# Optimization experiments

Hardware: AMD Instinct MI355X
Metric: run time of the kernel (lower is better)

## Reference

```python
import jax, jax.numpy as jnp
import numpy as np

D_MODEL = 1024
NUM_HEADS = 16


def setup_inputs() -> dict:
    key = jax.random.key(0)
    ks = jax.random.split(key, 5)
    sigma = (2.0 / (D_MODEL + D_MODEL)) ** 0.5
    def trunc(k):
        # truncated normal in [-3*sigma, 3*sigma], std sigma
        return sigma * jax.random.truncated_normal(k, -3.0, 3.0, (D_MODEL, D_MODEL), jnp.float32)
    x = jax.random.normal(ks[0], (4, 2048, D_MODEL), jnp.float32)
    return {
        "x": x,
        "W_Q": trunc(ks[1]),
        "W_K": trunc(ks[2]),
        "W_V": trunc(ks[3]),
        "W_O": trunc(ks[4]),
    }


def _mha(x, W_Q, W_K, W_V, W_O):
    B, S, D = x.shape
    H = NUM_HEADS
    dk = D // H
    # Linear stores W as (d_out, d_in); einsum '... d_in, d_out d_in -> ... d_out'
    Q = jnp.einsum('bsd,ed->bse', x, W_Q).reshape(B, S, H, dk).transpose(0, 2, 1, 3)
    K = jnp.einsum('bsd,ed->bse', x, W_K).reshape(B, S, H, dk).transpose(0, 2, 1, 3)
    V = jnp.einsum('bsd,ed->bse', x, W_V).reshape(B, S, H, dk).transpose(0, 2, 1, 3)
    scores = jnp.einsum('bhnd,bhmd->bhnm', Q, K) / jnp.sqrt(jnp.asarray(dk, x.dtype))
    causal = jnp.tril(jnp.ones((S, S), bool))
    scores = jnp.where(causal, scores, -jnp.inf)
    attn = jax.nn.softmax(scores, axis=-1)
    out = jnp.einsum('bhnm,bhmd->bhnd', attn, V)  # [B,H,S,dk]
    out = out.transpose(0, 2, 1, 3).reshape(B, S, D)
    return jnp.einsum('bsd,ed->bse', out, W_O)


def reference(x, W_Q, W_K, W_V, W_O):
    return _mha(x, W_Q, W_K, W_V, W_O)
```

## Files before the change

### kernel.cpp

```cpp
#include <hip/hip_runtime.h>
#include <hip/hip_bf16.h>
#include <stdint.h>


typedef unsigned short u16;
typedef short bf16x8 __attribute__((ext_vector_type(8)));
typedef float f32x4 __attribute__((ext_vector_type(4)));
typedef unsigned short u16x8 __attribute__((ext_vector_type(8)));

#define S_LEN 2048
#define DMODEL 1024
#define NH 16

__device__ __forceinline__ u16 f2bf(float f) {
    unsigned u = __builtin_bit_cast(unsigned, f);
    unsigned r = (u + 0x7fffu + ((u >> 16) & 1u)) >> 16;
    return (u16)r;
}

__device__ __forceinline__ float fast_exp2(float x) {
    return __builtin_amdgcn_exp2f(x);
}

__device__ __forceinline__ unsigned cvtpk_bf16(float lo, float hi_) {
    unsigned r;
    asm("v_cvt_pk_bf16_f32 %0, %1, %2" : "=v"(r) : "v"(lo), "v"(hi_));
    return r;
}

__device__ __forceinline__ void gll16(const void* g, void* s) {
    __builtin_amdgcn_global_load_lds((const __attribute__((address_space(1))) unsigned*)g,
                                     (__attribute__((address_space(3))) unsigned*)s, 16, 0, 0);
}

__global__ __launch_bounds__(256) void cast_all(
    const float* __restrict__ x, const float* __restrict__ wq, const float* __restrict__ wk,
    const float* __restrict__ wv, const float* __restrict__ wo,
    u16* __restrict__ xb, u16* __restrict__ wqkv, u16* __restrict__ wob, int nx) {
    const int NW = DMODEL * DMODEL;
    int i4 = (blockIdx.x * 256 + threadIdx.x) * 4;
    const float* src; u16* dst; int off;
    if (i4 < nx)             { src = x;  dst = xb;            off = i4; }
    else if (i4 < nx + NW)   { src = wq; dst = wqkv;          off = i4 - nx; }
    else if (i4 < nx + 2*NW) { src = wk; dst = wqkv + NW;     off = i4 - nx - NW; }
    else if (i4 < nx + 3*NW) { src = wv; dst = wqkv + 2*NW;   off = i4 - nx - 2*NW; }
    else                     { src = wo; dst = wob;           off = i4 - nx - 3*NW; }
    float4 v = *reinterpret_cast<const float4*>(src + off);
    ushort4 o4; o4.x = f2bf(v.x); o4.y = f2bf(v.y); o4.z = f2bf(v.z); o4.w = f2bf(v.w);
    *reinterpret_cast<ushort4*>(dst + off) = o4;
}

template <typename OUT>
__global__ __launch_bounds__(256) void gemm_bt(const u16* __restrict__ A, const u16* __restrict__ B,
                                               OUT* __restrict__ C, int M, int N, int K,
                                               int qcols, float qscale) {
    __shared__ u16 As[128 * 32];
    __shared__ u16 Bs[128 * 32];
    const int m0 = blockIdx.y * 128, n0 = blockIdx.x * 128;
    const int t = threadIdx.x, w = t >> 6, l = t & 63;
    const int wr = w >> 1, wc = w & 1;
    f32x4 acc[4][4] = {};

    const int srow = w * 16 + (l >> 2);
    const int scol = (l & 3) * 8;
    const u16* Ag = A + (size_t)(m0 + srow) * K + scol;
    const u16* Bg = B + (size_t)(n0 + srow) * K + scol;

    for (int k0 = 0; k0 < K; k0 += 32) {
        __syncthreads();
        gll16(Ag + k0,                  As + w * 512);
        gll16(Ag + (size_t)64 * K + k0, As + 2048 + w * 512);
        gll16(Bg + k0,                  Bs + w * 512);
        gll16(Bg + (size_t)64 * K + k0, Bs + 2048 + w * 512);
        __syncthreads();
        bf16x8 af[4], bfr[4];
#pragma unroll
        for (int mi = 0; mi < 4; mi++)
            af[mi] = *(const bf16x8*)&As[(wr * 64 + mi * 16 + (l & 15)) * 32 + (l >> 4) * 8];
#pragma unroll
        for (int ni = 0; ni < 4; ni++)
            bfr[ni] = *(const bf16x8*)&Bs[(wc * 64 + ni * 16 + (l & 15)) * 32 + (l >> 4) * 8];
#pragma unroll
        for (int mi = 0; mi < 4; mi++)
#pragma unroll
            for (int ni = 0; ni < 4; ni++)
                acc[mi][ni] = __builtin_amdgcn_mfma_f32_16x16x32_bf16(af[mi], bfr[ni], acc[mi][ni], 0, 0, 0);
    }
#pragma unroll
    for (int mi = 0; mi < 4; mi++)
#pragma unroll
        for (int ni = 0; ni < 4; ni++)
#pragma unroll
            for (int j = 0; j < 4; j++) {
                int r = m0 + wr * 64 + mi * 16 + (l >> 4) * 4 + j;
                int c = n0 + wc * 64 + ni * 16 + (l & 15);
                float v = acc[mi][ni][j];
                if (c < qcols) v *= qscale;
                if constexpr (__is_same(OUT, u16)) C[(size_t)r * N + c] = f2bf(v);
                else                               C[(size_t)r * N + c] = v;
            }
}

__global__ __launch_bounds__(256) void transpose_v(const u16* __restrict__ QKV, u16* __restrict__ VT) {
    __shared__ u16 tile[64 * 66];
    const int st = blockIdx.x, bh = blockIdx.y;
    const int b = bh >> 4, h = bh & 15;
    const int s0 = st * 64;
    const int t = threadIdx.x;
#pragma unroll
    for (int i = 0; i < 2; i++) {
        int cid = i * 256 + t;
        int srow = cid >> 3, c8 = cid & 7;
        u16x8 v = *(const u16x8*)&QKV[(size_t)(b * S_LEN + s0 + srow) * 3072 + 2048 + h * 64 + c8 * 8];
#pragma unroll
        for (int j = 0; j < 8; j++) tile[srow * 66 + c8 * 8 + j] = v[j];
    }
    __syncthreads();
#pragma unroll
    for (int i = 0; i < 2; i++) {
        int cid = i * 256 + t;
        int d = cid >> 3, sc8 = cid & 7;
        u16x8 o;
#pragma unroll
        for (int j = 0; j < 8; j++) o[j] = tile[(sc8 * 8 + j) * 66 + d];
        *(u16x8*)&VT[(size_t)(bh * 64 + d) * S_LEN + s0 + sc8 * 8] = o;
    }
}

__global__ __launch_bounds__(512, 4) void attn(const u16* __restrict__ QKV, const u16* __restrict__ VT,
                                               u16* __restrict__ O) {
    const int bh = blockIdx.x, p = blockIdx.y;
    const int b = bh >> 4, h = bh & 15;
    const int t = threadIdx.x, w = t >> 6, l = t & 63;
    const int q = l & 15, hi = l >> 4, s7 = q & 7;

    __shared__ u16 SM[2][2][64][64];
    __shared__ u16 PS[8][16][64];

    const int srow = t >> 3, sblk = t & 7;
    const int gs = (sblk ^ (srow & 7)) * 8;
    const u16* Kg = QKV + (size_t)(b * S_LEN + srow) * 3072 + 1024 + h * 64 + gs;
    const u16* Vg = VT + (size_t)(bh * 64 + srow) * S_LEN + gs;

    const int kA0 = q * 128 + ((hi ^ s7) << 4);
    const int kA1 = kA0 ^ 64;
    const char* smbase = (const char*)&SM[0][0][0][0];

    char* pbase = (char*)&PS[w][0][0];
    const int pw0 = q * 128 + ((((0 * 2) + (hi >> 1)) ^ s7) << 4) + ((hi & 1) << 3);
    const int pw1 = q * 128 + ((((1 * 2) + (hi >> 1)) ^ s7) << 4) + ((hi & 1) << 3);
    const int pw2 = q * 128 + ((((2 * 2) + (hi >> 1)) ^ s7) << 4) + ((hi & 1) << 3);
    const int pw3 = q * 128 + ((((3 * 2) + (hi >> 1)) ^ s7) << 4) + ((hi & 1) << 3);
    const int pr0 = q * 128 + (((0 * 4 + hi) ^ s7) << 4);
    const int pr1 = q * 128 + (((1 * 4 + hi) ^ s7) << 4);

#pragma unroll 1
    for (int part = 0; part < 2; ++part) {
        const int q128 = (part == 0 ? p : 15 - p) * 128;
        const int nt = q128 / 64 + 2;
        const int qglob = q128 + w * 16 + q;

        bf16x8 qf[2];
#pragma unroll
        for (int kk = 0; kk < 2; kk++)
            qf[kk] = *(const bf16x8*)&QKV[(size_t)(b * S_LEN + qglob) * 3072 + h * 64 + kk * 32 + hi * 8];

        f32x4 oacc[4] = {};
        float m_ = -1e30f, l_ = 0.f;

        gll16(Kg, (u16*)&SM[0][0][0][0] + t * 8);
        gll16(Vg, (u16*)&SM[0][1][0][0] + t * 8);
        __syncthreads();

        const u16* KgT = Kg + (size_t)64 * 3072;
        const u16* VgT = Vg + 64;

#pragma unroll 1
        for (int tt = 0; tt < nt; ++tt) {
            const int cur = tt & 1;
            if (tt + 1 < nt) {
                gll16(KgT, (u16*)&SM[cur ^ 1][0][0][0] + t * 8);
                gll16(VgT, (u16*)&SM[cur ^ 1][1][0][0] + t * 8);
                KgT += (size_t)64 * 3072;
                VgT += 64;
            }
            const int kv0 = tt * 64;
            if (q128 + w * 16 + 15 >= kv0) {
                const char* kb = smbase + cur * 16384;
                f32x4 sacc[4] = {};
#pragma unroll
                for (int kk = 0; kk < 2; kk++) {
                    const char* ka = kb + (kk ? kA1 : kA0);
#pragma unroll
                    for (int ni = 0; ni < 4; ni++) {
                        bf16x8 kf = *(const bf16x8*)(ka + ni * 2048);
                        sacc[ni] = __builtin_amdgcn_mfma_f32_16x16x32_bf16(kf, qf[kk], sacc[ni], 0, 0, 0);
                    }
                }
                const int r0 = qglob - kv0;
                if (r0 < 63) {
                    const int rth = r0 - hi * 4;
#pragma unroll
                    for (int ni = 0; ni < 4; ni++)
#pragma unroll
                        for (int j = 0; j < 4; j++)
                            if (ni * 16 + j > rth) sacc[ni][j] = -1e30f;
                }
                float x0 = fmaxf(fmaxf(sacc[0][0], sacc[0][1]), fmaxf(sacc[0][2], sacc[0][3]));
                float x1 = fmaxf(fmaxf(sacc[1][0], sacc[1][1]), fmaxf(sacc[1][2], sacc[1][3]));
                float x2 = fmaxf(fmaxf(sacc[2][0], sacc[2][1]), fmaxf(sacc[2][2], sacc[2][3]));
                float x3 = fmaxf(fmaxf(sacc[3][0], sacc[3][1]), fmaxf(sacc[3][2], sacc[3][3]));
                float pm = fmaxf(fmaxf(x0, x1), fmaxf(x2, x3));
                pm = fmaxf(pm, __shfl_xor(pm, 16, 64));
                pm = fmaxf(pm, __shfl_xor(pm, 32, 64));
                if (!__all(pm <= m_ + 8.0f)) {
                    float mnew = fmaxf(m_, pm);
                    float sc = fast_exp2(m_ - mnew);
                    m_ = mnew;
                    l_ *= sc;
#pragma unroll
                    for (int di = 0; di < 4; di++) oacc[di] *= sc;
                }
                float pv[4][4];
#pragma unroll
                for (int ni = 0; ni < 4; ni++)
#pragma unroll
                    for (int j = 0; j < 4; j++) pv[ni][j] = fast_exp2(sacc[ni][j] - m_);
                float ss = ((pv[0][0] + pv[0][1]) + (pv[0][2] + pv[0][3]))
                         + ((pv[1][0] + pv[1][1]) + (pv[1][2] + pv[1][3]))
                         + ((pv[2][0] + pv[2][1]) + (pv[2][2] + pv[2][3]))
                         + ((pv[3][0] + pv[3][1]) + (pv[3][2] + pv[3][3]));
                ss += __shfl_xor(ss, 16, 64);
                ss += __shfl_xor(ss, 32, 64);
                l_ += ss;
                *(uint2*)(pbase + pw0) = make_uint2(cvtpk_bf16(pv[0][0], pv[0][1]), cvtpk_bf16(pv[0][2], pv[0][3]));
                *(uint2*)(pbase + pw1) = make_uint2(cvtpk_bf16(pv[1][0], pv[1][1]), cvtpk_bf16(pv[1][2], pv[1][3]));
                *(uint2*)(pbase + pw2) = make_uint2(cvtpk_bf16(pv[2][0], pv[2][1]), cvtpk_bf16(pv[2][2], pv[2][3]));
                *(uint2*)(pbase + pw3) = make_uint2(cvtpk_bf16(pv[3][0], pv[3][1]), cvtpk_bf16(pv[3][2], pv[3][3]));
                bf16x8 pf0 = *(const bf16x8*)(pbase + pr0);
                bf16x8 pf1 = *(const bf16x8*)(pbase + pr1);
                const char* vb = kb + 8192;
#pragma unroll
                for (int kk = 0; kk < 2; kk++) {
                    const char* va = vb + (kk ? kA1 : kA0);
                    bf16x8 pf = kk ? pf1 : pf0;
#pragma unroll
                    for (int di = 0; di < 4; di++) {
                        bf16x8 vf = *(const bf16x8*)(va + di * 2048);
                        oacc[di] = __builtin_amdgcn_mfma_f32_16x16x32_bf16(vf, pf, oacc[di], 0, 0, 0);
                    }
                }
            }
            __syncthreads();
        }

        float inv = 1.0f / l_;
#pragma unroll
        for (int di = 0; di < 4; di++) {
            ushort4 o4;
            o4.x = f2bf(oacc[di][0] * inv);
            o4.y = f2bf(oacc[di][1] * inv);
            o4.z = f2bf(oacc[di][2] * inv);
            o4.w = f2bf(oacc[di][3] * inv);
            *(ushort4*)&O[(size_t)(b * S_LEN + qglob) * DMODEL + h * 64 + di * 16 + hi * 4] = o4;
        }
    }
}

extern "C" void kernel_launch(void* const* d_in, const int* in_sizes, int n_in,
                              void* d_out, int out_size, void* d_ws, size_t ws_size,
                              hipStream_t stream) {
    const float* x  = (const float*)d_in[0];
    const float* wq = (const float*)d_in[1];
    const float* wk = (const float*)d_in[2];
    const float* wv = (const float*)d_in[3];
    const float* wo = (const float*)d_in[4];
    const int nx = in_sizes[0];
    const int BS = nx / DMODEL;
    const int NW = DMODEL * DMODEL;

    u16* xb   = (u16*)d_ws;
    u16* wqkv = xb + (size_t)nx;
    u16* wob  = wqkv + (size_t)3 * NW;
    u16* qkv  = wob + (size_t)NW;
    u16* vt   = qkv + (size_t)BS * 3072;
    u16* ob   = vt + (size_t)nx;

    int ncast = (nx + 4 * NW) / 4 / 256;
    cast_all<<<ncast, 256, 0, stream>>>(x, wq, wk, wv, wo, xb, wqkv, wob, nx);

    const float QSC = 0.125f * 1.44269504088896f;
    gemm_bt<u16><<<dim3(3072 / 128, BS / 128), 256, 0, stream>>>(xb, wqkv, qkv, BS, 3072, DMODEL,
                                                                 DMODEL, QSC);

    transpose_v<<<dim3(S_LEN / 64, (BS / S_LEN) * NH), 256, 0, stream>>>(qkv, vt);

    attn<<<dim3((BS / S_LEN) * NH, 8), 512, 0, stream>>>(qkv, vt, ob);

    gemm_bt<float><<<dim3(DMODEL / 128, BS / 128), 256, 0, stream>>>(ob, wob, (float*)d_out, BS, DMODEL, DMODEL,
                                                                     0, 1.0f);
}
```

Measured before the change: 188.6 us.

## Fuse V transpose into QKV GEMM epilogue, widen GEMM K-tile with swizzle

The QKV GEMM now writes the V part directly in transposed layout through a small per-wave LDS staging buffer, which removes the separate transpose_v kernel and its extra read and write of V. The GEMM K-step grows from 32 to 64, with an XOR-swizzled LDS layout to avoid bank conflicts, halving the number of barrier pairs per tile. The attention kernel also wraps its MFMA blocks in s_setprio so those waves get issue priority. The costs are more LDS per GEMM block, which may lower occupancy, and the QKV buffer no longer holds V, which is fine because attention reads V only from vt.

```diff
diff --git a/kernel.cpp b/kernel.cpp
--- a/kernel.cpp
+++ b/kernel.cpp
@@ -53,77 +53,83 @@
 template <typename OUT>
 __global__ __launch_bounds__(256) void gemm_bt(const u16* __restrict__ A, const u16* __restrict__ B,
                                                OUT* __restrict__ C, int M, int N, int K,
-                                               int qcols, float qscale) {
-    __shared__ u16 As[128 * 32];
-    __shared__ u16 Bs[128 * 32];
+                                               int qcols, float qscale, u16* __restrict__ vt) {
+    __shared__ u16 As[128 * 64];
+    __shared__ u16 Bs[128 * 64];
+    __shared__ u16 Ts[4][16 * 72];
     const int m0 = blockIdx.y * 128, n0 = blockIdx.x * 128;
     const int t = threadIdx.x, w = t >> 6, l = t & 63;
+    const int hi = l >> 4;
     const int wr = w >> 1, wc = w & 1;
     f32x4 acc[4][4] = {};
 
-    const int srow = w * 16 + (l >> 2);
-    const int scol = (l & 3) * 8;
-    const u16* Ag = A + (size_t)(m0 + srow) * K + scol;
-    const u16* Bg = B + (size_t)(n0 + srow) * K + scol;
-
-    for (int k0 = 0; k0 < K; k0 += 32) {
+    const int lr = l >> 3;
+    const int lc = l & 7;
+    const int gcol = (lc ^ lr) * 8;
+    const u16* Ag = A + (size_t)(m0 + w * 32 + lr) * K + gcol;
+    const u16* Bg = B + (size_t)(n0 + w * 32 + lr) * K + gcol;
+
+    for (int k0 = 0; k0 < K; k0 += 64) {
         __syncthreads();
-        gll16(Ag + k0,                  As + w * 512);
-        gll16(Ag + (size_t)64 * K + k0, As + 2048 + w * 512);
-        gll16(Bg + k0,                  Bs + w * 512);
-        gll16(Bg + (size_t)64 * K + k0, Bs + 2048 + w * 512);
+#pragma unroll
+        for (int c = 0; c < 4; c++) {
+            gll16(Ag + (size_t)c * 8 * K + k0, As + w * 2048 + c * 512);
+            gll16(Bg + (size_t)c * 8 * K + k0, Bs + w * 2048 + c * 512);
+        }
         __syncthreads();
-        bf16x8 af[4], bfr[4];
+#pragma unroll
+        for (int kk = 0; kk < 2; kk++) {
+            bf16x8 af[4], bfr[4];
+#pragma unroll
+            for (int mi = 0; mi < 4; mi++)
+                af[mi] = *(const bf16x8*)&As[(wr * 64 + mi * 16 + (l & 15)) * 64 +
+                                             (((kk * 4 + hi) ^ (l & 7)) * 8)];
+#pragma unroll
+            for (int ni = 0; ni < 4; ni++)
+                bfr[ni] = *(const bf16x8*)&Bs[(wc * 64 + ni * 16 + (l & 15)) * 64 +
+                                              (((kk * 4 + hi) ^ (l & 7)) * 8)];
+#pragma unroll
+            for (int mi = 0; mi < 4; mi++)
+#pragma unroll
+                for (int ni = 0; ni < 4; ni++)
+                    acc[mi][ni] = __builtin_amdgcn_mfma_f32_16x16x32_bf16(af[mi], bfr[ni], acc[mi][ni], 0, 0, 0);
+        }
+    }
+
+    if (vt != nullptr && n0 >= 2048) {
+        const int mw = m0 + wr * 64;
+        const int bq = mw >> 11;
+        const int s0w = mw & (S_LEN - 1);
+        const int hd = ((n0 + wc * 64) - 2048) >> 6;
+        u16* tb = &Ts[w][0];
+#pragma unroll
+        for (int ni = 0; ni < 4; ni++) {
+#pragma unroll
+            for (int mi = 0; mi < 4; mi++) {
+                uint2 pk = make_uint2(cvtpk_bf16(acc[mi][ni][0], acc[mi][ni][1]),
+                                      cvtpk_bf16(acc[mi][ni][2], acc[mi][ni][3]));
+                *(uint2*)&tb[(l & 15) * 72 + mi * 16 + hi * 4] = pk;
+            }
+            bf16x8 r0 = *(const bf16x8*)&tb[(l & 15) * 72 + hi * 16];
+            bf16x8 r1 = *(const bf16x8*)&tb[(l & 15) * 72 + hi * 16 + 8];
+            size_t vrow = ((size_t)(bq * 16 + hd) * 64 + ni * 16 + (l & 15)) * S_LEN + s0w + hi * 16;
+            *(u16x8*)&vt[vrow]     = (u16x8)r0;
+            *(u16x8*)&vt[vrow + 8] = (u16x8)r1;
+        }
+    } else {
 #pragma unroll
         for (int mi = 0; mi < 4; mi++)
-            af[mi] = *(const bf16x8*)&As[(wr * 64 + mi * 16 + (l & 15)) * 32 + (l >> 4) * 8];
-#pragma unroll
-        for (int ni = 0; ni < 4; ni++)
-            bfr[ni] = *(const bf16x8*)&Bs[(wc * 64 + ni * 16 + (l & 15)) * 32 + (l >> 4) * 8];
-#pragma unroll
-        for (int mi = 0; mi < 4; mi++)
 #pragma unroll
             for (int ni = 0; ni < 4; ni++)
-                acc[mi][ni] = __builtin_amdgcn_mfma_f32_16x16x32_bf16(af[mi], bfr[ni], acc[mi][ni], 0, 0, 0);
-    }
-#pragma unroll
-    for (int mi = 0; mi < 4; mi++)
-#pragma unroll
-        for (int ni = 0; ni < 4; ni++)
-#pragma unroll
-            for (int j = 0; j < 4; j++) {
-                int r = m0 + wr * 64 + mi * 16 + (l >> 4) * 4 + j;
-                int c = n0 + wc * 64 + ni * 16 + (l & 15);
-                float v = acc[mi][ni][j];
-                if (c < qcols) v *= qscale;
-                if constexpr (__is_same(OUT, u16)) C[(size_t)r * N + c] = f2bf(v);
-                else                               C[(size_t)r * N + c] = v;
-            }
-}
-
-__global__ __launch_bounds__(256) void transpose_v(const u16* __restrict__ QKV, u16* __restrict__ VT) {
-    __shared__ u16 tile[64 * 66];
-    const int st = blockIdx.x, bh = blockIdx.y;
-    const int b = bh >> 4, h = bh & 15;
-    const int s0 = st * 64;
-    const int t = threadIdx.x;
-#pragma unroll
-    for (int i = 0; i < 2; i++) {
-        int cid = i * 256 + t;
-        int srow = cid >> 3, c8 = cid & 7;
-        u16x8 v = *(const u16x8*)&QKV[(size_t)(b * S_LEN + s0 + srow) * 3072 + 2048 + h * 64 + c8 * 8];
-#pragma unroll
-        for (int j = 0; j < 8; j++) tile[srow * 66 + c8 * 8 + j] = v[j];
-    }
-    __syncthreads();
-#pragma unroll
-    for (int i = 0; i < 2; i++) {
-        int cid = i * 256 + t;
-        int d = cid >> 3, sc8 = cid & 7;
-        u16x8 o;
-#pragma unroll
-        for (int j = 0; j < 8; j++) o[j] = tile[(sc8 * 8 + j) * 66 + d];
-        *(u16x8*)&VT[(size_t)(bh * 64 + d) * S_LEN + s0 + sc8 * 8] = o;
+#pragma unroll
+                for (int j = 0; j < 4; j++) {
+                    int r = m0 + wr * 64 + mi * 16 + hi * 4 + j;
+                    int c = n0 + wc * 64 + ni * 16 + (l & 15);
+                    float v = acc[mi][ni][j];
+                    if (c < qcols) v *= qscale;
+                    if constexpr (__is_same(OUT, u16)) C[(size_t)r * N + c] = f2bf(v);
+                    else                               C[(size_t)r * N + c] = v;
+                }
     }
 }
 
@@ -188,6 +194,7 @@
             if (q128 + w * 16 + 15 >= kv0) {
                 const char* kb = smbase + cur * 16384;
                 f32x4 sacc[4] = {};
+                __builtin_amdgcn_s_setprio(1);
 #pragma unroll
                 for (int kk = 0; kk < 2; kk++) {
                     const char* ka = kb + (kk ? kA1 : kA0);
@@ -197,6 +204,7 @@
                         sacc[ni] = __builtin_amdgcn_mfma_f32_16x16x32_bf16(kf, qf[kk], sacc[ni], 0, 0, 0);
                     }
                 }
+                __builtin_amdgcn_s_setprio(0);
                 const int r0 = qglob - kv0;
                 if (r0 < 63) {
                     const int rth = r0 - hi * 4;
@@ -240,6 +248,7 @@
                 bf16x8 pf0 = *(const bf16x8*)(pbase + pr0);
                 bf16x8 pf1 = *(const bf16x8*)(pbase + pr1);
                 const char* vb = kb + 8192;
+                __builtin_amdgcn_s_setprio(1);
 #pragma unroll
                 for (int kk = 0; kk < 2; kk++) {
                     const char* va = vb + (kk ? kA1 : kA0);
@@ -250,6 +259,7 @@
                         oacc[di] = __builtin_amdgcn_mfma_f32_16x16x32_bf16(vf, pf, oacc[di], 0, 0, 0);
                     }
                 }
+                __builtin_amdgcn_s_setprio(0);
             }
             __syncthreads();
         }
@@ -291,12 +301,10 @@
 
     const float QSC = 0.125f * 1.44269504088896f;
     gemm_bt<u16><<<dim3(3072 / 128, BS / 128), 256, 0, stream>>>(xb, wqkv, qkv, BS, 3072, DMODEL,
-                                                                 DMODEL, QSC);
-
-    transpose_v<<<dim3(S_LEN / 64, (BS / S_LEN) * NH), 256, 0, stream>>>(qkv, vt);
+                                                                 DMODEL, QSC, vt);
 
     attn<<<dim3((BS / S_LEN) * NH, 8), 512, 0, stream>>>(qkv, vt, ob);
 
     gemm_bt<float><<<dim3(DMODEL / 128, BS / 128), 256, 0, stream>>>(ob, wob, (float*)d_out, BS, DMODEL, DMODEL,
-                                                                     0, 1.0f);
-}
+                                                                     0, 1.0f, nullptr);
+}
```

Measured after the change: 168.8 us. 1.12x faster.
